# Performance work log

Measured on AMD Instinct MI355X. Metric: run time of the kernel, lower is better.

The kernel has to match this reference:

```python
import jax, jax.numpy as jnp
import numpy as np

D_MODEL = 256
D_INNER = 512   # expand=2 * d_model
D_STATE = 16
D_CONV = 4
DT_RANK = 16    # ceil(d_model/16)
N_BLOCKS = 5
BATCH = 8192
INPUT_DIM = 2048
NUM_CLASSES = 8


def setup_inputs() -> dict:
    key = jax.random.key(0)
    ks = jax.random.split(key, 10)
    rn = lambda k, shape, s: jax.random.normal(k, shape, jnp.float32) * s
    inp = {}
    inp['x'] = rn(ks[0], (BATCH, INPUT_DIM), 1.0)
    # preprocess Linear(input_dim, 256)
    inp['W_pre'] = rn(ks[1], (D_MODEL, INPUT_DIM), 0.02)
    inp['b_pre'] = jnp.zeros((D_MODEL,), jnp.float32)
    # per-block Mamba params, stacked over N_BLOCKS
    inp['in_proj_w'] = rn(ks[2], (N_BLOCKS, 2 * D_INNER, D_MODEL), 0.02)
    inp['conv_w'] = rn(ks[3], (N_BLOCKS, D_INNER, 1, D_CONV), 0.1)   # depthwise, groups=d_inner
    inp['conv_b'] = jnp.zeros((N_BLOCKS, D_INNER), jnp.float32)
    inp['x_proj_w'] = rn(ks[4], (N_BLOCKS, DT_RANK + 2 * D_STATE, D_INNER), 0.02)
    inp['dt_proj_w'] = rn(ks[5], (N_BLOCKS, D_INNER, DT_RANK), 0.1)
    inp['dt_proj_b'] = rn(ks[6], (N_BLOCKS, D_INNER), 0.1)
    # S4D-real init: A = 1..d_state, A_log = log(A)
    A = jnp.tile(jnp.arange(1, D_STATE + 1, dtype=jnp.float32)[None, None, :], (N_BLOCKS, D_INNER, 1))
    inp['A_log'] = jnp.log(A)
    inp['D'] = jnp.ones((N_BLOCKS, D_INNER), jnp.float32)
    inp['out_proj_w'] = rn(ks[7], (N_BLOCKS, D_MODEL, D_INNER), 0.02)
    inp['ln_g'] = jnp.ones((D_MODEL,), jnp.float32)
    inp['ln_b'] = jnp.zeros((D_MODEL,), jnp.float32)
    inp['W_cls'] = rn(ks[8], (NUM_CLASSES, D_MODEL), 0.02)
    inp['b_cls'] = jnp.zeros((NUM_CLASSES,), jnp.float32)
    return inp


def _mamba(x, in_w, cw, cb, xw, dtw, dtb, Alog, Dp, ow):
    # x: (B, L, d_model)
    B, L, _ = x.shape
    xz = jnp.einsum('bld,ed->ble', x, in_w)            # (B, L, 2*d_inner)
    xi, z = jnp.split(xz, 2, axis=-1)
    # causal depthwise conv1d over the sequence axis
    xt = xi.transpose(0, 2, 1)                         # (B, d_inner, L)
    xc = jax.lax.conv_general_dilated(
        xt, cw, window_strides=(1,), padding=[(D_CONV - 1, 0)],
        dimension_numbers=('NCH', 'OIH', 'NCH'), feature_group_count=D_INNER)
    xi = jax.nn.silu((xc + cb[None, :, None]).transpose(0, 2, 1))   # (B, L, d_inner)
    xdbl = jnp.einsum('bld,ed->ble', xi, xw)           # (B, L, dt_rank + 2*d_state)
    dt, Bm, Cm = jnp.split(xdbl, [DT_RANK, DT_RANK + D_STATE], axis=-1)
    dt = jax.nn.softplus(jnp.einsum('blr,dr->bld', dt, dtw) + dtb)  # (B, L, d_inner)
    A = -jnp.exp(Alog)                                  # (d_inner, d_state)
    dA = jnp.exp(dt[..., None] * A)                     # (B, L, d_inner, d_state)
    dBx = dt[..., None] * Bm[:, :, None, :] * xi[..., None]

    def step(h, t):
        dA_t, dBx_t, C_t = t
        h = dA_t * h + dBx_t                            # (B, d_inner, d_state)
        return h, jnp.einsum('bds,bs->bd', h, C_t)

    h0 = jnp.zeros((B, D_INNER, D_STATE), x.dtype)
    _, ys = jax.lax.scan(step, h0, (dA.swapaxes(0, 1), dBx.swapaxes(0, 1), Cm.swapaxes(0, 1)))
    y = ys.swapaxes(0, 1) + xi * Dp                     # (B, L, d_inner)
    y = y * jax.nn.silu(z)
    return jnp.einsum('bld,ed->ble', y, ow)             # (B, L, d_model)


def reference(x, W_pre, b_pre, in_proj_w, conv_w, conv_b, x_proj_w, dt_proj_w,
              dt_proj_b, A_log, D, out_proj_w, ln_g, ln_b, W_cls, b_cls):
    # dropout is identity in eval mode
    h = (x @ W_pre.T + b_pre)[:, None, :]               # (B, 1, 256)
    for i in range(N_BLOCKS):
        h = h + _mamba(h, in_proj_w[i], conv_w[i], conv_b[i], x_proj_w[i],
                       dt_proj_w[i], dt_proj_b[i], A_log[i], D[i], out_proj_w[i])
    mu = h.mean(-1, keepdims=True)
    var = ((h - mu) ** 2).mean(-1, keepdims=True)
    hn = (h - mu) * jax.lax.rsqrt(var + 1e-5) * ln_g + ln_b
    return hn[:, 0, :] @ W_cls.T + b_cls                # (B, num_classes)
```

## Files before the change

### kernel.cpp

```cpp
#include <hip/hip_runtime.h>
#include <hip/hip_bf16.h>

typedef __attribute__((ext_vector_type(8))) short bf16x8;
typedef __attribute__((ext_vector_type(4))) short s16x4;
typedef __attribute__((ext_vector_type(4))) float f32x4;
typedef __attribute__((ext_vector_type(4))) float float4v;

static __device__ __forceinline__ unsigned short f2b(float f) {
  unsigned int u = __builtin_bit_cast(unsigned int, f);
  u += 0x7fffu + ((u >> 16) & 1u);
  return (unsigned short)(u >> 16);
}
static __device__ __forceinline__ float b2f(unsigned short s) {
  unsigned int u = ((unsigned int)s) << 16;
  return __builtin_bit_cast(float, u);
}
static __device__ __forceinline__ float fsilu(float x) {
  float e = __builtin_amdgcn_exp2f(-1.44269504f * x);
  return x * __builtin_amdgcn_rcpf(1.f + e);
}
static __device__ __forceinline__ float fsoftplus(float a) {
  if (a > 20.f) return a;
  float t = __builtin_amdgcn_exp2f(1.44269504f * a);
  return 0.69314718f * __builtin_amdgcn_logf(1.f + t);
}
static __device__ __forceinline__ void gl16(const void* g, void* l) {
  __builtin_amdgcn_global_load_lds(
      (const __attribute__((address_space(1))) unsigned int*)g,
      (__attribute__((address_space(3))) unsigned int*)l, 16, 0, 0);
}
template <int N>
static __device__ __forceinline__ void waitv() {
  if constexpr (N == 0) asm volatile("s_waitcnt vmcnt(0)" ::: "memory");
  else if constexpr (N == 1) asm volatile("s_waitcnt vmcnt(1)" ::: "memory");
  else if constexpr (N == 2) asm volatile("s_waitcnt vmcnt(2)" ::: "memory");
  else if constexpr (N == 3) asm volatile("s_waitcnt vmcnt(3)" ::: "memory");
  else if constexpr (N == 4) asm volatile("s_waitcnt vmcnt(4)" ::: "memory");
  else if constexpr (N == 5) asm volatile("s_waitcnt vmcnt(5)" ::: "memory");
  else if constexpr (N == 6) asm volatile("s_waitcnt vmcnt(6)" ::: "memory");
  else if constexpr (N == 8) asm volatile("s_waitcnt vmcnt(8)" ::: "memory");
}
static __device__ __forceinline__ void lgkm_bar() {
  asm volatile("s_waitcnt lgkmcnt(0)" ::: "memory");
  __builtin_amdgcn_s_barrier();
}

template <int TM, int TN>
__global__ __launch_bounds__(256) void gemm_pl(
    const unsigned short* __restrict__ A, const unsigned short* __restrict__ W,
    int N, int K, int GY,
    const float* __restrict__ p0, float* __restrict__ of,
    unsigned short* __restrict__ ob) {
  constexpr int FM = TM / 32, FN = TN / 32;
  constexpr int IA = TM / 64, IW = TN / 64;
  constexpr int LPT = IA + IW;
  __shared__ __align__(16) unsigned short As[4][TM * 32];
  __shared__ __align__(16) unsigned short Ws[4][TN * 32];

  const int t = threadIdx.x, lane = t & 63, wave = t >> 6;
  const int lr = lane & 15;
  const int q = gridDim.x >> 3;
  const int s = (blockIdx.x & 7) * q + (blockIdx.x >> 3);
  const int bm = (s / GY) * TM, bn = (s % GY) * TN;
  const int wr = (wave >> 1) * (TM / 2), wc = (wave & 1) * (TN / 2);

  f32x4 acc[FM][FN];
#pragma unroll
  for (int i = 0; i < FM; ++i)
#pragma unroll
    for (int j = 0; j < FN; ++j) acc[i][j] = (f32x4){0.f, 0.f, 0.f, 0.f};

  const unsigned short* agB =
      A + (long)(bm + wave * (TM / 4) + (lane >> 2)) * K +
      ((lane & 3) ^ ((lane >> 3) & 3)) * 8;
  const unsigned short* wgB =
      W + (long)(bn + wave * (TN / 4) + (lane >> 2)) * K +
      ((lane & 3) ^ ((lane >> 3) & 3)) * 8;

  auto STAGE = [&](int k0, int b) {
#pragma unroll
    for (int j = 0; j < IA; ++j)
      gl16(agB + k0 + (long)j * 16 * K, &As[b][(wave * (TM / 4) + j * 16) * 32]);
#pragma unroll
    for (int j = 0; j < IW; ++j)
      gl16(wgB + k0 + (long)j * 16 * K, &Ws[b][(wave * (TN / 4) + j * 16) * 32]);
  };

  auto COMPUTE = [&](int b) {
    bf16x8 af[FM], bg[FN];
    const int sw = ((lane >> 4) ^ ((lane >> 1) & 3)) * 8;
#pragma unroll
    for (int m = 0; m < FM; ++m)
      af[m] = *(const bf16x8*)&As[b][(wr + m * 16 + lr) * 32 + sw];
#pragma unroll
    for (int n = 0; n < FN; ++n)
      bg[n] = *(const bf16x8*)&Ws[b][(wc + n * 16 + lr) * 32 + sw];
    __builtin_amdgcn_s_setprio(1);
#pragma unroll
    for (int m = 0; m < FM; ++m)
#pragma unroll
      for (int n = 0; n < FN; ++n)
        acc[m][n] = __builtin_amdgcn_mfma_f32_16x16x32_bf16(af[m], bg[n],
                                                            acc[m][n], 0, 0, 0);
    __builtin_amdgcn_s_setprio(0);
  };

  const int NT = K >> 5;
  STAGE(0, 0);
  STAGE(32, 1);
  for (int tt = 0; tt < NT; ++tt) {
    if (tt + 2 < NT) {
      STAGE((tt + 2) << 5, (tt + 2) & 3);
      waitv<2 * LPT>();
    } else if (tt + 1 < NT) {
      waitv<LPT>();
    } else {
      waitv<0>();
    }
    __builtin_amdgcn_s_barrier();
    COMPUTE(tt & 3);
    __builtin_amdgcn_sched_barrier(0);
  }

  const int m0 = bm + wr + (lane >> 4) * 4;
  const int n0 = bn + wc + lr;
#pragma unroll
  for (int mi = 0; mi < FM; ++mi)
#pragma unroll
    for (int ni = 0; ni < FN; ++ni) {
      const int n = n0 + ni * 16;
#pragma unroll
      for (int r = 0; r < 4; ++r) {
        const int m = m0 + mi * 16 + r;
        float v = acc[mi][ni][r] + p0[n];
        of[(long)m * N + n] = v;
        ob[(long)m * N + n] = f2b(v);
      }
    }
}

__global__ __launch_bounds__(512) void mamba5(
    const unsigned short* __restrict__ hb0, const float* __restrict__ h0,
    const unsigned short* __restrict__ inwb,
    const unsigned short* __restrict__ xwpb,
    const unsigned short* __restrict__ dtwpb,
    const unsigned short* __restrict__ owb,
    const float* __restrict__ conv_b, const float* __restrict__ dt_b,
    const float* __restrict__ Dp,
    const float* __restrict__ ln_g, const float* __restrict__ ln_b,
    const float* __restrict__ Wc, const float* __restrict__ bc,
    float* __restrict__ out) {
  __shared__ __align__(16) unsigned short SMEM[81216];
  unsigned short* XiL = SMEM;
  unsigned short* SzL = SMEM + 16384;
  unsigned short* Ring = SMEM + 32768;
  unsigned short* HLr = SMEM + 65536;
  float* Dxl = (float*)(SMEM + 73728);
  float* BCl = (float*)(SMEM + 78080);
  float* Par = (float*)(SMEM + 78144);

  const int t = threadIdx.x, lane = t & 63, w = t >> 6;
  const int lr = lane & 15, lg = lane >> 4;
  const int bm = blockIdx.x * 32;
  const int m04 = lg * 4;
  const int rg16 = (w >> 2) * 16;
  const int cg32 = (w & 3) * 32;
  const int strow = lane >> 2;
  const int stc = (lane & 3) ^ ((strow >> 1) & 3);

#pragma unroll
  for (int j = 0; j < 2; ++j) {
    const int i = w * 2 + j;
    const int row = 2 * i + (lane >> 5);
    const int c = (lane & 31) ^ (row & 7);
    gl16(hb0 + (long)(bm + row) * 256 + c * 8, HLr + i * 512);
  }
  float hres[2][2][4];
#pragma unroll
  for (int ng = 0; ng < 2; ++ng)
#pragma unroll
    for (int n = 0; n < 2; ++n)
#pragma unroll
      for (int r = 0; r < 4; ++r)
        hres[ng][n][r] = h0[(long)(bm + rg16 + m04 + r) * 256 + ng * 128 +
                            cg32 + n * 16 + lr];
  waitv<0>();
  __builtin_amdgcn_s_barrier();

  for (int blk = 0; blk < 5; ++blk) {
    const unsigned short* inw = inwb + (long)blk * 1024 * 256;
    const unsigned short* xwp = xwpb + (long)blk * 64 * 512;
    const unsigned short* dtwp = dtwpb + (long)blk * 512 * 32;
    const unsigned short* ow = owb + (long)blk * 256 * 512;
    const float* cbv = conv_b + blk * 512;
    const float* dtbv = dt_b + blk * 512;
    const float* Dv = Dp + blk * 512;

    auto STAGE1 = [&](int tt, int slot) {
      const int nt = tt >> 3, kq = tt & 7;
      gl16(inw + (long)(nt * 128 + w * 16 + strow) * 256 + kq * 32 + stc * 8,
           Ring + slot * 4096 + w * 512);
    };
    if (w < 6) {
      const float* ps = (w < 2) ? cbv + (w & 1) * 256
                      : (w < 4) ? dtbv + (w & 1) * 256
                                : Dv + (w & 1) * 256;
      gl16(ps + lane * 4, (unsigned short*)Par + w * 512);
    }
    STAGE1(0, 0); STAGE1(1, 1); STAGE1(2, 2); STAGE1(3, 3);
    STAGE1(4, 4); STAGE1(5, 5); STAGE1(6, 6);
    f32x4 acc1[2];
#pragma unroll
    for (int tt = 0; tt < 64; ++tt) {
      if (tt <= 57) waitv<6>();
      else if (tt == 58) waitv<5>();
      else if (tt == 59) waitv<4>();
      else if (tt == 60) waitv<3>();
      else if (tt == 61) waitv<2>();
      else if (tt == 62) waitv<1>();
      else waitv<0>();
      __builtin_amdgcn_s_barrier();
      if (tt + 7 < 64) STAGE1(tt + 7, (tt + 7) & 7);
      __builtin_amdgcn_sched_barrier(0);
      const int nt = tt >> 3, kq = tt & 7;
      if (kq == 0) {
#pragma unroll
        for (int n = 0; n < 2; ++n) {
          const int c = nt * 128 + cg32 + n * 16 + lr;
          const float cb = (nt < 4) ? Par[c] : 0.f;
          acc1[n] = (f32x4){cb, cb, cb, cb};
        }
      }
      const unsigned short* Bs = Ring + (tt & 7) * 4096;
      const int ar = rg16 + lr;
      bf16x8 af = *(const bf16x8*)
          &HLr[ar * 256 + (((kq * 4 + lg) ^ (ar & 7)) * 8)];
      bf16x8 bg[2];
#pragma unroll
      for (int n = 0; n < 2; ++n) {
        const int rb = cg32 + n * 16 + lr;
        bg[n] = *(const bf16x8*)&Bs[rb * 32 + ((lg ^ ((rb >> 1) & 3)) * 8)];
      }
      __builtin_amdgcn_s_setprio(1);
#pragma unroll
      for (int n = 0; n < 2; ++n)
        acc1[n] = __builtin_amdgcn_mfma_f32_16x16x32_bf16(af, bg[n], acc1[n],
                                                          0, 0, 0);
      __builtin_amdgcn_s_setprio(0);
      if (kq == 7) {
#pragma unroll
        for (int n = 0; n < 2; ++n) {
          const int c = nt * 128 + cg32 + n * 16 + lr;
#pragma unroll
          for (int r = 0; r < 4; ++r) {
            const int row = rg16 + m04 + r;
            const float v = fsilu(acc1[n][r]);
            if (nt < 4)
              XiL[row * 512 + (((c >> 3) ^ (row & 7)) * 8) + (c & 7)] = f2b(v);
            else
              SzL[row * 512 + (c - 512)] = f2b(v);
          }
        }
      }
      __builtin_amdgcn_sched_barrier(0);
    }
    lgkm_bar();

#pragma unroll
    for (int j = 0; j < 8; ++j) {
      const int i = w * 8 + j;
      gl16(xwp + (long)i * 512 + (lane ^ (i & 7)) * 8, Ring + i * 512);
    }
    waitv<0>();
    __builtin_amdgcn_s_barrier();
    {
      const int fm2 = w & 1, fn2 = w >> 1;
      const int ar = fm2 * 16 + lr, rb = fn2 * 16 + lr;
      f32x4 a2 = {0.f, 0.f, 0.f, 0.f};
      __builtin_amdgcn_s_setprio(1);
#pragma unroll
      for (int kc = 0; kc < 16; ++kc) {
        bf16x8 af = *(const bf16x8*)
            &XiL[ar * 512 + (((kc * 4 + lg) ^ (lr & 7)) * 8)];
        bf16x8 bg = *(const bf16x8*)
            &Ring[rb * 512 + (((kc * 4 + lg) ^ (lr & 7)) * 8)];
        a2 = __builtin_amdgcn_mfma_f32_16x16x32_bf16(af, bg, a2, 0, 0, 0);
      }
      __builtin_amdgcn_s_setprio(0);
#pragma unroll
      for (int r = 0; r < 4; ++r)
        Dxl[(fm2 * 16 + m04 + r) * 68 + fn2 * 16 + lr] = a2[r];
    }
    lgkm_bar();

#pragma unroll
    for (int j = 0; j < 4; ++j) {
      const int u = w * 4 + j;
      const int row = u * 16 + (lane >> 2);
      const int c = (lane & 3) ^ (row & 3);
      gl16(dtwp + (long)row * 32 + c * 8, Ring + u * 512);
    }
    if (t < 32) {
      float bc2 = 0.f;
      const float* dx = &Dxl[t * 68];
#pragma unroll
      for (int s2 = 0; s2 < 16; ++s2) bc2 += dx[16 + s2] * dx[32 + s2];
      BCl[t] = bc2;
    }
    bf16x8 afdt;
    {
      const float* dx = &Dxl[((w & 1) * 16 + lr) * 68 + lg * 8];
#pragma unroll
      for (int e = 0; e < 8; ++e) afdt[e] = (short)f2b(dx[e]);
    }
    waitv<0>();
    lgkm_bar();

    {
      const int fn4 = w >> 1, m04b = (w & 1) * 16 + m04;
#pragma unroll
      for (int tt = 0; tt < 8; ++tt) {
        const int d = tt * 64 + fn4 * 16 + lr;
        bf16x8 bg = *(const bf16x8*)&Ring[d * 32 + ((lg ^ (d & 3)) * 8)];
        f32x4 da = __builtin_amdgcn_mfma_f32_16x16x32_bf16(
            afdt, bg, (f32x4){0.f, 0.f, 0.f, 0.f}, 0, 0, 0);
        const float dbv = Par[512 + d], dvv = Par[1024 + d];
#pragma unroll
        for (int r = 0; r < 4; ++r) {
          const int row = m04b + r;
          const float dtv = fsoftplus(da[r] + dbv);
          const int xoff = row * 512 + (((d >> 3) ^ (row & 7)) * 8) + (d & 7);
          const float y = b2f(XiL[xoff]) * (dtv * BCl[row] + dvv) *
                          b2f(SzL[row * 512 + d]);
          XiL[xoff] = f2b(y);
        }
      }
    }
    lgkm_bar();

    auto STAGE5 = [&](int tt, int slot) {
      const int ng = tt >> 4, kq = tt & 15;
      gl16(ow + (long)(ng * 128 + w * 16 + strow) * 512 + kq * 32 + stc * 8,
           Ring + slot * 4096 + w * 512);
    };
    STAGE5(0, 0); STAGE5(1, 1); STAGE5(2, 2); STAGE5(3, 3);
    STAGE5(4, 4); STAGE5(5, 5); STAGE5(6, 6);
    f32x4 acc5[2];
#pragma unroll
    for (int tt = 0; tt < 32; ++tt) {
      if (tt <= 25) waitv<6>();
      else if (tt == 26) waitv<5>();
      else if (tt == 27) waitv<4>();
      else if (tt == 28) waitv<3>();
      else if (tt == 29) waitv<2>();
      else if (tt == 30) waitv<1>();
      else waitv<0>();
      __builtin_amdgcn_s_barrier();
      if (tt + 7 < 32) STAGE5(tt + 7, (tt + 7) & 7);
      __builtin_amdgcn_sched_barrier(0);
      const int ng = tt >> 4, kq = tt & 15;
      if (kq == 0) {
        acc5[0] = (f32x4){0.f, 0.f, 0.f, 0.f};
        acc5[1] = (f32x4){0.f, 0.f, 0.f, 0.f};
      }
      const unsigned short* Bs = Ring + (tt & 7) * 4096;
      const int ar = rg16 + lr;
      bf16x8 af = *(const bf16x8*)
          &XiL[ar * 512 + (((kq * 4 + lg) ^ (ar & 7)) * 8)];
      bf16x8 bg[2];
#pragma unroll
      for (int n = 0; n < 2; ++n) {
        const int rb = cg32 + n * 16 + lr;
        bg[n] = *(const bf16x8*)&Bs[rb * 32 + ((lg ^ ((rb >> 1) & 3)) * 8)];
      }
      __builtin_amdgcn_s_setprio(1);
#pragma unroll
      for (int n = 0; n < 2; ++n)
        acc5[n] = __builtin_amdgcn_mfma_f32_16x16x32_bf16(af, bg[n], acc5[n],
                                                          0, 0, 0);
      __builtin_amdgcn_s_setprio(0);
      if (kq == 15) {
#pragma unroll
        for (int n = 0; n < 2; ++n) {
          const int col = ng * 128 + cg32 + n * 16 + lr;
#pragma unroll
          for (int r = 0; r < 4; ++r) {
            const int row = rg16 + m04 + r;
            const float v = acc5[n][r] + hres[ng][n][r];
            hres[ng][n][r] = v;
            HLr[row * 256 + (((col >> 3) ^ (row & 7)) * 8) + (col & 7)] =
                f2b(v);
          }
        }
      }
      __builtin_amdgcn_sched_barrier(0);
    }
    lgkm_bar();
  }

  {
    float* Rf = (float*)Ring;
#pragma unroll
    for (int ng = 0; ng < 2; ++ng)
#pragma unroll
      for (int n = 0; n < 2; ++n)
#pragma unroll
        for (int r = 0; r < 4; ++r)
          Rf[(rg16 + m04 + r) * 256 + ng * 128 + cg32 + n * 16 + lr] =
              hres[ng][n][r];
    lgkm_bar();
#pragma unroll
    for (int rr = 0; rr < 4; ++rr) {
      const int row = w * 4 + rr;
      float4v v = ((const float4v*)(Rf + row * 256))[lane];
      float s = v[0] + v[1] + v[2] + v[3];
#pragma unroll
      for (int o = 32; o; o >>= 1) s += __shfl_xor(s, o);
      const float mu = s * (1.f / 256.f);
      float d0 = v[0] - mu, d1 = v[1] - mu, d2 = v[2] - mu, d3 = v[3] - mu;
      float qq = d0 * d0 + d1 * d1 + d2 * d2 + d3 * d3;
#pragma unroll
      for (int o = 32; o; o >>= 1) qq += __shfl_xor(qq, o);
      const float rs = rsqrtf(qq * (1.f / 256.f) + 1e-5f);
      const float4v gv = ((const float4v*)ln_g)[lane];
      const float4v bv = ((const float4v*)ln_b)[lane];
      float hn[4];
      hn[0] = d0 * rs * gv[0] + bv[0];
      hn[1] = d1 * rs * gv[1] + bv[1];
      hn[2] = d2 * rs * gv[2] + bv[2];
      hn[3] = d3 * rs * gv[3] + bv[3];
      float lgt[8];
#pragma unroll
      for (int o = 0; o < 8; ++o) {
        const float4v wv = ((const float4v*)(Wc + o * 256))[lane];
        float p = hn[0] * wv[0] + hn[1] * wv[1] + hn[2] * wv[2] + hn[3] * wv[3];
#pragma unroll
        for (int x = 32; x; x >>= 1) p += __shfl_xor(p, x);
        lgt[o] = p;
      }
      if (lane == 0) {
#pragma unroll
        for (int o = 0; o < 8; ++o)
          out[(long)(bm + row) * 8 + o] = lgt[o] + bc[o];
      }
    }
  }
}

__global__ __launch_bounds__(256) void castx(const float* __restrict__ s,
                                             unsigned short* __restrict__ d) {
  const int n4 = (8192 * 2048) / 4;
  for (int i = blockIdx.x * 256 + threadIdx.x; i < n4; i += gridDim.x * 256) {
    float4v v = ((const float4v*)s)[i];
    s16x4 o;
    o[0] = (short)f2b(v[0]); o[1] = (short)f2b(v[1]);
    o[2] = (short)f2b(v[2]); o[3] = (short)f2b(v[3]);
    ((s16x4*)d)[i] = o;
  }
}

__global__ __launch_bounds__(256) void precast(
    const float* __restrict__ wpre, const float* __restrict__ inw,
    const float* __restrict__ ow, const float* __restrict__ xw,
    const float* __restrict__ dtw, const float* __restrict__ cw,
    unsigned short* __restrict__ wpreb, unsigned short* __restrict__ inwb,
    unsigned short* __restrict__ owb, unsigned short* __restrict__ xwpb,
    unsigned short* __restrict__ dtwpb) {
  const int S0 = 524288;
  const int S1 = S0 + 1310720;
  const int S2 = S1 + 655360;
  const int S3 = S2 + 163840;
  const int S4 = S3 + 81920;
  int i4 = (blockIdx.x * 256 + threadIdx.x) * 4;
  if (i4 >= S4) return;
  float4v v = {0.f, 0.f, 0.f, 0.f};
  unsigned short* dst;
  if (i4 < S0) {
    v = *(const float4v*)(wpre + i4);
    dst = wpreb + i4;
  } else if (i4 < S1) {
    int o = i4 - S0;
    v = *(const float4v*)(inw + o);
    int b = o >> 18, row = (o >> 8) & 1023;
    if (row < 512) {
      float c3 = cw[(b * 512 + row) * 4 + 3];
      v[0] *= c3; v[1] *= c3; v[2] *= c3; v[3] *= c3;
    }
    dst = inwb + o;
  } else if (i4 < S2) {
    int o = i4 - S1;
    v = *(const float4v*)(ow + o);
    dst = owb + o;
  } else if (i4 < S3) {
    int o = i4 - S2;
    dst = xwpb + o;
    int k = o & 511, j = (o >> 9) & 63, b = o >> 15;
    if (j < 48) v = *(const float4v*)(xw + ((long)(b * 48 + j)) * 512 + k);
  } else {
    int o = i4 - S3;
    dst = dtwpb + o;
    int k = o & 31, dd = o >> 5;
    if (k < 16) v = *(const float4v*)(dtw + (long)dd * 16 + k);
  }
  s16x4 sv;
  sv[0] = (short)f2b(v[0]); sv[1] = (short)f2b(v[1]);
  sv[2] = (short)f2b(v[2]); sv[3] = (short)f2b(v[3]);
  *(s16x4*)dst = sv;
}

extern "C" void kernel_launch(void* const* d_in, const int* in_sizes, int n_in,
                              void* d_out, int out_size, void* d_ws,
                              size_t ws_size, hipStream_t stream) {
  const float* x      = (const float*)d_in[0];
  const float* W_pre  = (const float*)d_in[1];
  const float* b_pre  = (const float*)d_in[2];
  const float* in_w   = (const float*)d_in[3];
  const float* conv_w = (const float*)d_in[4];
  const float* conv_b = (const float*)d_in[5];
  const float* x_w    = (const float*)d_in[6];
  const float* dt_w   = (const float*)d_in[7];
  const float* dt_b   = (const float*)d_in[8];
  const float* Dp     = (const float*)d_in[10];
  const float* out_w  = (const float*)d_in[11];
  const float* ln_g   = (const float*)d_in[12];
  const float* ln_b   = (const float*)d_in[13];
  const float* W_cls  = (const float*)d_in[14];
  const float* b_cls  = (const float*)d_in[15];
  float* out = (float*)d_out;

  char* w = (char*)d_ws;
  unsigned short* wpreb = (unsigned short*)w; w += 256 * 2048 * 2;
  unsigned short* inwb  = (unsigned short*)w; w += 5 * 1024 * 256 * 2;
  unsigned short* xwpb  = (unsigned short*)w; w += 5 * 64 * 512 * 2;
  unsigned short* owb   = (unsigned short*)w; w += 5 * 256 * 512 * 2;
  unsigned short* dtwpb = (unsigned short*)w; w += 5 * 512 * 32 * 2;
  float*          h     = (float*)w;          w += 8192 * 256 * 4;
  unsigned short* hb    = (unsigned short*)w; w += 8192 * 256 * 2;
  unsigned short* xb    = (unsigned short*)w; w += 8192 * 2048 * 2;

  precast<<<2672, 256, 0, stream>>>(W_pre, in_w, out_w, x_w, dt_w, conv_w,
                                    wpreb, inwb, owb, xwpb, dtwpb);
  castx<<<2048, 256, 0, stream>>>(x, xb);

  gemm_pl<128, 64><<<256, 256, 0, stream>>>(
      xb, wpreb, 256, 2048, 4, b_pre, h, hb);

  mamba5<<<256, 512, 0, stream>>>(hb, h, inwb, xwpb, dtwpb, owb,
                                  conv_b, dt_b, Dp,
                                  ln_g, ln_b, W_cls, b_cls, out);
}
```

Before: 192.2 us.

## Prefetch next block's in_proj tiles and x_proj weights across stage boundaries

Keeps the global-to-LDS load pipeline full across stage boundaries in the fused Mamba kernel. The out_proj loop's tail iterations now issue the first in_proj tiles of the next block. The in_proj loop's tail prefetches x_proj weight rows, and the per-block parameter vectors (conv bias, dt bias, D) are loaded ahead for the next block. This removes pipeline drain and refill bubbles between stages, in exchange for more complex vmcnt accounting. The conv bias is now added in the epilogue instead of being used to initialise the accumulator, so Par is not read before its load has landed.

Result: slower. 217.6 us (+13.3%).

```diff
diff --git a/kernel.cpp b/kernel.cpp
--- a/kernel.cpp
+++ b/kernel.cpp
@@ -38,6 +38,7 @@
   else if constexpr (N == 4) asm volatile("s_waitcnt vmcnt(4)" ::: "memory");
   else if constexpr (N == 5) asm volatile("s_waitcnt vmcnt(5)" ::: "memory");
   else if constexpr (N == 6) asm volatile("s_waitcnt vmcnt(6)" ::: "memory");
+  else if constexpr (N == 7) asm volatile("s_waitcnt vmcnt(7)" ::: "memory");
   else if constexpr (N == 8) asm volatile("s_waitcnt vmcnt(8)" ::: "memory");
 }
 static __device__ __forceinline__ void lgkm_bar() {
@@ -167,6 +168,7 @@
   const int cg32 = (w & 3) * 32;
   const int strow = lane >> 2;
   const int stc = (lane & 3) ^ ((strow >> 1) & 3);
+  const int seg = (w < 6) ? w : (w - 2);
 
 #pragma unroll
   for (int j = 0; j < 2; ++j) {
@@ -187,49 +189,46 @@
   waitv<0>();
   __builtin_amdgcn_s_barrier();
 
+#pragma unroll
+  for (int j = 0; j < 7; ++j)
+    gl16(inwb + (long)(w * 16 + strow) * 256 + j * 32 + stc * 8,
+         Ring + j * 4096 + w * 512);
+  {
+    const float* ps = (seg < 2) ? conv_b + (seg & 1) * 256
+                    : (seg < 4) ? dt_b + (seg & 1) * 256
+                                : Dp + (seg & 1) * 256;
+    gl16(ps + lane * 4, (unsigned short*)Par + seg * 512);
+  }
+
   for (int blk = 0; blk < 5; ++blk) {
     const unsigned short* inw = inwb + (long)blk * 1024 * 256;
     const unsigned short* xwp = xwpb + (long)blk * 64 * 512;
     const unsigned short* dtwp = dtwpb + (long)blk * 512 * 32;
     const unsigned short* ow = owb + (long)blk * 256 * 512;
-    const float* cbv = conv_b + blk * 512;
-    const float* dtbv = dt_b + blk * 512;
-    const float* Dv = Dp + blk * 512;
-
-    auto STAGE1 = [&](int tt, int slot) {
+
+    auto STAGE1 = [&](int tt) {
       const int nt = tt >> 3, kq = tt & 7;
       gl16(inw + (long)(nt * 128 + w * 16 + strow) * 256 + kq * 32 + stc * 8,
-           Ring + slot * 4096 + w * 512);
+           Ring + (tt & 7) * 4096 + w * 512);
     };
-    if (w < 6) {
-      const float* ps = (w < 2) ? cbv + (w & 1) * 256
-                      : (w < 4) ? dtbv + (w & 1) * 256
-                                : Dv + (w & 1) * 256;
-      gl16(ps + lane * 4, (unsigned short*)Par + w * 512);
-    }
-    STAGE1(0, 0); STAGE1(1, 1); STAGE1(2, 2); STAGE1(3, 3);
-    STAGE1(4, 4); STAGE1(5, 5); STAGE1(6, 6);
     f32x4 acc1[2];
 #pragma unroll
     for (int tt = 0; tt < 64; ++tt) {
-      if (tt <= 57) waitv<6>();
-      else if (tt == 58) waitv<5>();
-      else if (tt == 59) waitv<4>();
-      else if (tt == 60) waitv<3>();
-      else if (tt == 61) waitv<2>();
-      else if (tt == 62) waitv<1>();
-      else waitv<0>();
+      if (tt < 7) waitv<7>();
+      else waitv<6>();
       __builtin_amdgcn_s_barrier();
-      if (tt + 7 < 64) STAGE1(tt + 7, (tt + 7) & 7);
+      if (tt + 7 < 64) {
+        STAGE1(tt + 7);
+      } else {
+        const int p = tt - 57;
+        gl16(xwp + (long)(p * 8 + w) * 512 + (lane ^ ((p * 8 + w) & 7)) * 8,
+             Ring + (p * 8 + w) * 512);
+      }
       __builtin_amdgcn_sched_barrier(0);
       const int nt = tt >> 3, kq = tt & 7;
       if (kq == 0) {
-#pragma unroll
-        for (int n = 0; n < 2; ++n) {
-          const int c = nt * 128 + cg32 + n * 16 + lr;
-          const float cb = (nt < 4) ? Par[c] : 0.f;
-          acc1[n] = (f32x4){cb, cb, cb, cb};
-        }
+        acc1[0] = (f32x4){0.f, 0.f, 0.f, 0.f};
+        acc1[1] = (f32x4){0.f, 0.f, 0.f, 0.f};
       }
       const unsigned short* Bs = Ring + (tt & 7) * 4096;
       const int ar = rg16 + lr;
@@ -251,10 +250,11 @@
 #pragma unroll
         for (int n = 0; n < 2; ++n) {
           const int c = nt * 128 + cg32 + n * 16 + lr;
+          const float cb = (nt < 4) ? Par[c] : 0.f;
 #pragma unroll
           for (int r = 0; r < 4; ++r) {
             const int row = rg16 + m04 + r;
-            const float v = fsilu(acc1[n][r]);
+            const float v = fsilu(acc1[n][r] + cb);
             if (nt < 4)
               XiL[row * 512 + (((c >> 3) ^ (row & 7)) * 8) + (c & 7)] = f2b(v);
             else
@@ -266,11 +266,8 @@
     }
     lgkm_bar();
 
-#pragma unroll
-    for (int j = 0; j < 8; ++j) {
-      const int i = w * 8 + j;
-      gl16(xwp + (long)i * 512 + (lane ^ (i & 7)) * 8, Ring + i * 512);
-    }
+    gl16(xwp + (long)(56 + w) * 512 + (lane ^ ((56 + w) & 7)) * 8,
+         Ring + (56 + w) * 512);
     waitv<0>();
     __builtin_amdgcn_s_barrier();
     {
@@ -338,25 +335,36 @@
     }
     lgkm_bar();
 
-    auto STAGE5 = [&](int tt, int slot) {
+    auto STAGE5 = [&](int tt) {
       const int ng = tt >> 4, kq = tt & 15;
       gl16(ow + (long)(ng * 128 + w * 16 + strow) * 512 + kq * 32 + stc * 8,
-           Ring + slot * 4096 + w * 512);
+           Ring + (tt & 7) * 4096 + w * 512);
     };
-    STAGE5(0, 0); STAGE5(1, 1); STAGE5(2, 2); STAGE5(3, 3);
-    STAGE5(4, 4); STAGE5(5, 5); STAGE5(6, 6);
+    STAGE5(0); STAGE5(1); STAGE5(2); STAGE5(3);
+    STAGE5(4); STAGE5(5); STAGE5(6);
+    const unsigned short* inw_n = inwb + (long)(blk + 1) * 1024 * 256;
     f32x4 acc5[2];
 #pragma unroll
     for (int tt = 0; tt < 32; ++tt) {
-      if (tt <= 25) waitv<6>();
-      else if (tt == 26) waitv<5>();
-      else if (tt == 27) waitv<4>();
-      else if (tt == 28) waitv<3>();
-      else if (tt == 29) waitv<2>();
-      else if (tt == 30) waitv<1>();
-      else waitv<0>();
+      if (blk < 4) {
+        waitv<6>();
+      } else {
+        if (tt <= 25) waitv<6>();
+        else if (tt == 26) waitv<5>();
+        else if (tt == 27) waitv<4>();
+        else if (tt == 28) waitv<3>();
+        else if (tt == 29) waitv<2>();
+        else if (tt == 30) waitv<1>();
+        else waitv<0>();
+      }
       __builtin_amdgcn_s_barrier();
-      if (tt + 7 < 32) STAGE5(tt + 7, (tt + 7) & 7);
+      if (tt + 7 < 32) {
+        STAGE5(tt + 7);
+      } else if (blk < 4) {
+        const int j = tt - 25;
+        gl16(inw_n + (long)(w * 16 + strow) * 256 + j * 32 + stc * 8,
+             Ring + j * 4096 + w * 512);
+      }
       __builtin_amdgcn_sched_barrier(0);
       const int ng = tt >> 4, kq = tt & 15;
       if (kq == 0) {
@@ -396,6 +404,13 @@
       __builtin_amdgcn_sched_barrier(0);
     }
     lgkm_bar();
+
+    if (blk < 4) {
+      const float* ps = (seg < 2) ? conv_b + (blk + 1) * 512 + (seg & 1) * 256
+                      : (seg < 4) ? dt_b + (blk + 1) * 512 + (seg & 1) * 256
+                                  : Dp + (blk + 1) * 512 + (seg & 1) * 256;
+      gl16(ps + lane * 4, (unsigned short*)Par + seg * 512);
+    }
   }
 
   {
```
